# Kernel optimization log

Measured on AMD Instinct MI355X. Metric: run time of the kernel, lower is better.

## Reference

```python
import jax, jax.numpy as jnp
import numpy as np

N, T, H, D = 32, 2048, 1024, 384

def setup_inputs() -> dict:
    key = jax.random.key(0)
    k1, k2, k3, k4, k5 = jax.random.split(key, 5)
    scale_h = 1.0 / np.sqrt(H)
    scale_d = 1.0 / np.sqrt(D)
    return {
        "gru_output": jax.random.normal(k1, (N, T, H), dtype=jnp.float32),
        "condition": jax.random.normal(k2, (N, D), dtype=jnp.float32),
        "W_h": jax.random.normal(k3, (H, H), dtype=jnp.float32) * scale_h,
        "W_c": jax.random.normal(k4, (D, H), dtype=jnp.float32) * scale_d,
        "bias": jnp.zeros((H,), dtype=jnp.float32),
        "v": jax.random.normal(k5, (H,), dtype=jnp.float32) * scale_h,
    }

def reference(gru_output, condition, W_h, W_c, bias, v):
    # h_proj: (N, T, H); c_proj: (N, 1, H)
    h_proj = jnp.einsum("nth,hk->ntk", gru_output, W_h)
    c_proj = jnp.einsum("nd,dk->nk", condition, W_c)[:, None, :]
    energy = jnp.tanh(h_proj + c_proj + bias)          # (N, T, H)
    scores = jnp.einsum("ntk,k->nt", energy, v)        # (N, T)
    weights = jax.nn.softmax(scores, axis=-1)          # (N, T)
    context = jnp.einsum("nth,nt->nh", gru_output, weights)  # (N, H)
    return context
```

## Files before the change

### kernel.cpp

```cpp
#include <hip/hip_runtime.h>
#include <hip/hip_bf16.h>

#define N_B 32
#define T_S 2048
#define H_D 1024
#define D_C 384
#define NT  (N_B * T_S)

typedef __attribute__((ext_vector_type(8))) short bf16x8;
typedef __attribute__((ext_vector_type(4))) float f32x4;

__device__ __forceinline__ ushort f2bf(float f) {
    union { float f; unsigned u; } x; x.f = f;
    unsigned u = x.u;
    unsigned r = (u + 0x7FFFu + ((u >> 16) & 1u)) >> 16;
    return (ushort)r;
}

__device__ __forceinline__ float fast_tanh(float x) {
    float e = __expf(2.0f * x);
    return 1.0f - 2.0f / (e + 1.0f);
}

__global__ __launch_bounds__(256) void transpose_kernel(
    const float* __restrict__ W, ushort* __restrict__ Wt)
{
    __shared__ ushort tile[64 * 66];
    const int bx = blockIdx.x & 15;
    const int by = blockIdx.x >> 4;
    const int t = threadIdx.x;
    #pragma unroll
    for (int i = 0; i < 16; ++i) {
        int idx = t + i * 256;
        int r = idx >> 6, c = idx & 63;
        tile[r * 66 + c] = f2bf(W[(size_t)(by * 64 + r) * H_D + bx * 64 + c]);
    }
    __syncthreads();
    #pragma unroll
    for (int i = 0; i < 16; ++i) {
        int idx = t + i * 256;
        int r = idx >> 6, c = idx & 63;
        Wt[(size_t)(bx * 64 + r) * H_D + by * 64 + c] = tile[c * 66 + r];
    }
}

__global__ __launch_bounds__(256) void cproj_kernel(
    const float* __restrict__ cond, const float* __restrict__ Wc,
    const float* __restrict__ bias, float* __restrict__ cproj)
{
    const int idx = blockIdx.x * 256 + threadIdx.x;
    const int n = idx >> 10, k = idx & 1023;
    float acc = bias[k];
    const float* cp = cond + n * D_C;
    for (int d = 0; d < D_C; ++d)
        acc = fmaf(cp[d], Wc[(size_t)d * H_D + k], acc);
    cproj[idx] = acc;
}

#define LDSS 40
__global__ __launch_bounds__(256) void gemm_score_kernel(
    const float* __restrict__ gru, const ushort* __restrict__ Wt,
    const float* __restrict__ cproj, const float* __restrict__ v,
    float* __restrict__ scores)
{
    __shared__ __align__(16) ushort As[128 * LDSS];
    __shared__ __align__(16) ushort Bt[128 * LDSS];
    const int kb = blockIdx.x;
    const int mb = blockIdx.y;
    const int m0 = mb * 128;
    const int nbatch = mb >> 4;
    const int t = threadIdx.x;
    const int lane = t & 63, wave = t >> 6;
    const int wm = wave & 1, wn = wave >> 1;
    const int q = lane >> 4, ln = lane & 15;

    f32x4 acc[4][4];
    #pragma unroll
    for (int i = 0; i < 4; ++i)
        #pragma unroll
        for (int j = 0; j < 4; ++j)
            acc[i][j] = (f32x4){0.f, 0.f, 0.f, 0.f};

    for (int h0 = 0; h0 < H_D; h0 += 32) {
        if (h0) __syncthreads();
        #pragma unroll
        for (int i = 0; i < 4; ++i) {
            int f = t + i * 256;
            int row = f >> 3, c4 = f & 7;
            const float4 val = *(const float4*)(gru + (size_t)(m0 + row) * H_D + h0 + c4 * 4);
            ushort4 o;
            o.x = f2bf(val.x); o.y = f2bf(val.y); o.z = f2bf(val.z); o.w = f2bf(val.w);
            *(ushort4*)(&As[row * LDSS + c4 * 4]) = o;
        }
        #pragma unroll
        for (int i = 0; i < 2; ++i) {
            int f = t + i * 256;
            int n = f >> 2, c = f & 3;
            uint4 wv = *(const uint4*)(Wt + (size_t)(kb * 128 + n) * H_D + h0 + c * 8);
            *(uint4*)(&Bt[n * LDSS + c * 8]) = wv;
        }
        __syncthreads();
        bf16x8 a[4], b[4];
        #pragma unroll
        for (int i = 0; i < 4; ++i)
            a[i] = *(const bf16x8*)(&As[(wm * 64 + i * 16 + ln) * LDSS + q * 8]);
        #pragma unroll
        for (int j = 0; j < 4; ++j)
            b[j] = *(const bf16x8*)(&Bt[(wn * 64 + j * 16 + ln) * LDSS + q * 8]);
        #pragma unroll
        for (int i = 0; i < 4; ++i)
            #pragma unroll
            for (int j = 0; j < 4; ++j)
                acc[i][j] = __builtin_amdgcn_mfma_f32_16x16x32_bf16(a[i], b[j], acc[i][j], 0, 0, 0);
    }

    float cpv[4], vv[4];
    const float* cpn = cproj + nbatch * H_D;
    #pragma unroll
    for (int j = 0; j < 4; ++j) {
        int col = kb * 128 + wn * 64 + j * 16 + ln;
        cpv[j] = cpn[col];
        vv[j] = v[col];
    }
    #pragma unroll
    for (int i = 0; i < 4; ++i) {
        float s0 = 0.f, s1 = 0.f, s2 = 0.f, s3 = 0.f;
        #pragma unroll
        for (int j = 0; j < 4; ++j) {
            s0 += fast_tanh(acc[i][j][0] + cpv[j]) * vv[j];
            s1 += fast_tanh(acc[i][j][1] + cpv[j]) * vv[j];
            s2 += fast_tanh(acc[i][j][2] + cpv[j]) * vv[j];
            s3 += fast_tanh(acc[i][j][3] + cpv[j]) * vv[j];
        }
        #pragma unroll
        for (int off = 1; off < 16; off <<= 1) {
            s0 += __shfl_xor(s0, off);
            s1 += __shfl_xor(s1, off);
            s2 += __shfl_xor(s2, off);
            s3 += __shfl_xor(s3, off);
        }
        if (ln == 0) {
            int mrow = m0 + wm * 64 + i * 16 + q * 4;
            atomicAdd(&scores[mrow + 0], s0);
            atomicAdd(&scores[mrow + 1], s1);
            atomicAdd(&scores[mrow + 2], s2);
            atomicAdd(&scores[mrow + 3], s3);
        }
    }
}

__global__ __launch_bounds__(256) void softmax_kernel(
    const float* __restrict__ scores, float* __restrict__ weights)
{
    const int n = blockIdx.x;
    const int t = threadIdx.x;
    __shared__ float red[256];
    float sv[8];
    float m = -1e30f;
    #pragma unroll
    for (int i = 0; i < 8; ++i) {
        sv[i] = scores[n * T_S + i * 256 + t];
        m = fmaxf(m, sv[i]);
    }
    red[t] = m; __syncthreads();
    for (int s = 128; s > 0; s >>= 1) {
        if (t < s) red[t] = fmaxf(red[t], red[t + s]);
        __syncthreads();
    }
    const float mx = red[0];
    __syncthreads();
    float sum = 0.f;
    #pragma unroll
    for (int i = 0; i < 8; ++i) { sv[i] = __expf(sv[i] - mx); sum += sv[i]; }
    red[t] = sum; __syncthreads();
    for (int s = 128; s > 0; s >>= 1) {
        if (t < s) red[t] += red[t + s];
        __syncthreads();
    }
    const float inv = 1.0f / red[0];
    #pragma unroll
    for (int i = 0; i < 8; ++i) weights[n * T_S + i * 256 + t] = sv[i] * inv;
}

__global__ __launch_bounds__(256) void context_kernel(
    const float* __restrict__ gru, const float* __restrict__ weights,
    float* __restrict__ out)
{
    const int tb = blockIdx.x;
    const int n  = blockIdx.y;
    const int t4 = threadIdx.x;
    float4 acc = make_float4(0.f, 0.f, 0.f, 0.f);
    const float* wp = weights + n * T_S + tb * 256;
    const float* gp = gru + (size_t)(n * T_S + tb * 256) * H_D + t4 * 4;
    for (int tt = 0; tt < 256; ++tt) {
        float w = wp[tt];
        float4 gv = *(const float4*)(gp + (size_t)tt * H_D);
        acc.x += w * gv.x; acc.y += w * gv.y;
        acc.z += w * gv.z; acc.w += w * gv.w;
    }
    float* op = out + n * H_D + t4 * 4;
    atomicAdd(op + 0, acc.x);
    atomicAdd(op + 1, acc.y);
    atomicAdd(op + 2, acc.z);
    atomicAdd(op + 3, acc.w);
}

extern "C" void kernel_launch(void* const* d_in, const int* in_sizes, int n_in,
                              void* d_out, int out_size, void* d_ws, size_t ws_size,
                              hipStream_t stream)
{
    const float* gru  = (const float*)d_in[0];
    const float* cond = (const float*)d_in[1];
    const float* W_h  = (const float*)d_in[2];
    const float* W_c  = (const float*)d_in[3];
    const float* bias = (const float*)d_in[4];
    const float* v    = (const float*)d_in[5];
    float* out = (float*)d_out;

    char* ws = (char*)d_ws;
    ushort* Wt     = (ushort*)ws;
    float*  cproj  = (float*)(ws + (2u << 20));
    float*  scores = (float*)(ws + (2u << 20) + (128u << 10));
    float*  wts    = (float*)(ws + (2u << 20) + (384u << 10));

    hipMemsetAsync(scores, 0, NT * sizeof(float), stream);
    hipMemsetAsync(out, 0, N_B * H_D * sizeof(float), stream);

    transpose_kernel<<<256, 256, 0, stream>>>(W_h, Wt);
    cproj_kernel<<<128, 256, 0, stream>>>(cond, W_c, bias, cproj);
    gemm_score_kernel<<<dim3(8, 512), 256, 0, stream>>>(gru, Wt, cproj, v, scores);
    softmax_kernel<<<N_B, 256, 0, stream>>>(scores, wts);
    context_kernel<<<dim3(8, N_B), 256, 0, stream>>>(gru, wts, out);
}
```

Measured before the change: 650.6 us.

## Pre-convert activations to bf16 and load GEMM tiles directly into LDS

Adds a pass that converts gru_output to bf16 once into the workspace. The GEMM then streams both operands with global_load_lds straight into shared memory, so the fp32 data is no longer re-read and re-converted by every one of the 8 column blocks. Per-block score partials go to separate slices that the softmax kernel sums, replacing the atomics and the memset. The cost is an extra full read and write of the activations plus a 128 MB workspace requirement; without that workspace the code falls back to the old path. The unpadded LDS layout may also cause bank conflicts.

```diff
diff --git a/kernel.cpp b/kernel.cpp
--- a/kernel.cpp
+++ b/kernel.cpp
@@ -9,6 +9,7 @@
 
 typedef __attribute__((ext_vector_type(8))) short bf16x8;
 typedef __attribute__((ext_vector_type(4))) float f32x4;
+typedef __attribute__((ext_vector_type(8))) unsigned short u16x8;
 
 __device__ __forceinline__ ushort f2bf(float f) {
     union { float f; unsigned u; } x; x.f = f;
@@ -22,6 +23,24 @@
     return 1.0f - 2.0f / (e + 1.0f);
 }
 
+__device__ __forceinline__ void gl2lds16(const void* g, void* l) {
+    __builtin_amdgcn_global_load_lds(
+        (const __attribute__((address_space(1))) void*)g,
+        (__attribute__((address_space(3))) void*)l, 16, 0, 0);
+}
+
+__global__ __launch_bounds__(256) void convert_kernel(
+    const float* __restrict__ g, ushort* __restrict__ gb)
+{
+    const size_t base = ((size_t)blockIdx.x * 256 + threadIdx.x) * 8;
+    float4 v0 = *(const float4*)(g + base);
+    float4 v1 = *(const float4*)(g + base + 4);
+    u16x8 o;
+    o[0] = f2bf(v0.x); o[1] = f2bf(v0.y); o[2] = f2bf(v0.z); o[3] = f2bf(v0.w);
+    o[4] = f2bf(v1.x); o[5] = f2bf(v1.y); o[6] = f2bf(v1.z); o[7] = f2bf(v1.w);
+    *(u16x8*)(gb + base) = o;
+}
+
 __global__ __launch_bounds__(256) void transpose_kernel(
     const float* __restrict__ W, ushort* __restrict__ Wt)
 {
@@ -50,11 +69,110 @@
 {
     const int idx = blockIdx.x * 256 + threadIdx.x;
     const int n = idx >> 10, k = idx & 1023;
-    float acc = bias[k];
+    float a0 = bias[k], a1 = 0.f, a2 = 0.f, a3 = 0.f;
     const float* cp = cond + n * D_C;
-    for (int d = 0; d < D_C; ++d)
-        acc = fmaf(cp[d], Wc[(size_t)d * H_D + k], acc);
-    cproj[idx] = acc;
+    for (int d = 0; d < D_C; d += 4) {
+        a0 = fmaf(cp[d + 0], Wc[(size_t)(d + 0) * H_D + k], a0);
+        a1 = fmaf(cp[d + 1], Wc[(size_t)(d + 1) * H_D + k], a1);
+        a2 = fmaf(cp[d + 2], Wc[(size_t)(d + 2) * H_D + k], a2);
+        a3 = fmaf(cp[d + 3], Wc[(size_t)(d + 3) * H_D + k], a3);
+    }
+    cproj[idx] = (a0 + a1) + (a2 + a3);
+}
+
+__global__ __launch_bounds__(256) void gemm2_kernel(
+    const ushort* __restrict__ Ab, const ushort* __restrict__ Wt,
+    const float* __restrict__ cproj, const float* __restrict__ v,
+    float* __restrict__ spart)
+{
+    __shared__ __align__(16) ushort As[128 * 32];
+    __shared__ __align__(16) ushort Bs[128 * 32];
+    __shared__ float red[2][2][4][16];
+    const int kb = blockIdx.x;
+    const int mb = blockIdx.y;
+    const int m0 = mb * 128;
+    const int nbatch = mb >> 4;
+    const int t = threadIdx.x;
+    const int lane = t & 63, wave = t >> 6;
+    const int wm = wave & 1, wn = wave >> 1;
+    const int q = lane >> 4, ln = lane & 15;
+
+    const ushort* ag0 = Ab + (size_t)(m0 + (t >> 2)) * H_D + (t & 3) * 8;
+    const ushort* ag1 = Ab + (size_t)(m0 + 64 + (t >> 2)) * H_D + (t & 3) * 8;
+    const ushort* bg0 = Wt + (size_t)(kb * 128 + (t >> 2)) * H_D + (t & 3) * 8;
+    const ushort* bg1 = Wt + (size_t)(kb * 128 + 64 + (t >> 2)) * H_D + (t & 3) * 8;
+    ushort* asd0 = As + wave * 512;
+    ushort* asd1 = As + 2048 + wave * 512;
+    ushort* bsd0 = Bs + wave * 512;
+    ushort* bsd1 = Bs + 2048 + wave * 512;
+
+    f32x4 acc[4][4];
+    #pragma unroll
+    for (int i = 0; i < 4; ++i)
+        #pragma unroll
+        for (int j = 0; j < 4; ++j)
+            acc[i][j] = (f32x4){0.f, 0.f, 0.f, 0.f};
+
+    for (int h0 = 0; h0 < H_D; h0 += 32) {
+        if (h0) __syncthreads();
+        gl2lds16(ag0 + h0, asd0);
+        gl2lds16(ag1 + h0, asd1);
+        gl2lds16(bg0 + h0, bsd0);
+        gl2lds16(bg1 + h0, bsd1);
+        __syncthreads();
+        bf16x8 a[4], b[4];
+        #pragma unroll
+        for (int i = 0; i < 4; ++i)
+            a[i] = *(const bf16x8*)(&As[(wm * 64 + i * 16 + ln) * 32 + q * 8]);
+        #pragma unroll
+        for (int j = 0; j < 4; ++j)
+            b[j] = *(const bf16x8*)(&Bs[(wn * 64 + j * 16 + ln) * 32 + q * 8]);
+        #pragma unroll
+        for (int i = 0; i < 4; ++i)
+            #pragma unroll
+            for (int j = 0; j < 4; ++j)
+                acc[i][j] = __builtin_amdgcn_mfma_f32_16x16x32_bf16(a[i], b[j], acc[i][j], 0, 0, 0);
+    }
+
+    float cpv[4], vv[4];
+    const float* cpn = cproj + nbatch * H_D;
+    #pragma unroll
+    for (int j = 0; j < 4; ++j) {
+        int col = kb * 128 + wn * 64 + j * 16 + ln;
+        cpv[j] = cpn[col];
+        vv[j] = v[col];
+    }
+    #pragma unroll
+    for (int i = 0; i < 4; ++i) {
+        float s0 = 0.f, s1 = 0.f, s2 = 0.f, s3 = 0.f;
+        #pragma unroll
+        for (int j = 0; j < 4; ++j) {
+            s0 += fast_tanh(acc[i][j][0] + cpv[j]) * vv[j];
+            s1 += fast_tanh(acc[i][j][1] + cpv[j]) * vv[j];
+            s2 += fast_tanh(acc[i][j][2] + cpv[j]) * vv[j];
+            s3 += fast_tanh(acc[i][j][3] + cpv[j]) * vv[j];
+        }
+        #pragma unroll
+        for (int off = 1; off < 16; off <<= 1) {
+            s0 += __shfl_xor(s0, off);
+            s1 += __shfl_xor(s1, off);
+            s2 += __shfl_xor(s2, off);
+            s3 += __shfl_xor(s3, off);
+        }
+        if (ln == 0) {
+            red[wm][wn][i][q * 4 + 0] = s0;
+            red[wm][wn][i][q * 4 + 1] = s1;
+            red[wm][wn][i][q * 4 + 2] = s2;
+            red[wm][wn][i][q * 4 + 3] = s3;
+        }
+    }
+    __syncthreads();
+    if (t < 128) {
+        int wm2 = t >> 6, idx = t & 63;
+        int i2 = idx >> 4, qr = idx & 15;
+        float val = red[wm2][0][i2][qr] + red[wm2][1][i2][qr];
+        spart[(size_t)kb * NT + m0 + wm2 * 64 + idx] = val;
+    }
 }
 
 #define LDSS 40
@@ -147,6 +265,43 @@
             atomicAdd(&scores[mrow + 3], s3);
         }
     }
+}
+
+__global__ __launch_bounds__(256) void softmax8_kernel(
+    const float* __restrict__ spart, float* __restrict__ weights)
+{
+    const int n = blockIdx.x;
+    const int t = threadIdx.x;
+    __shared__ float red[256];
+    float sv[8];
+    float m = -1e30f;
+    #pragma unroll
+    for (int i = 0; i < 8; ++i) {
+        int mrow = n * T_S + i * 256 + t;
+        float s = 0.f;
+        #pragma unroll
+        for (int kb = 0; kb < 8; ++kb) s += spart[(size_t)kb * NT + mrow];
+        sv[i] = s;
+        m = fmaxf(m, s);
+    }
+    red[t] = m; __syncthreads();
+    for (int s = 128; s > 0; s >>= 1) {
+        if (t < s) red[t] = fmaxf(red[t], red[t + s]);
+        __syncthreads();
+    }
+    const float mx = red[0];
+    __syncthreads();
+    float sum = 0.f;
+    #pragma unroll
+    for (int i = 0; i < 8; ++i) { sv[i] = __expf(sv[i] - mx); sum += sv[i]; }
+    red[t] = sum; __syncthreads();
+    for (int s = 128; s > 0; s >>= 1) {
+        if (t < s) red[t] += red[t + s];
+        __syncthreads();
+    }
+    const float inv = 1.0f / red[0];
+    #pragma unroll
+    for (int i = 0; i < 8; ++i) weights[n * T_S + i * 256 + t] = sv[i] * inv;
 }
 
 __global__ __launch_bounds__(256) void softmax_kernel(
@@ -218,17 +373,39 @@
     float* out = (float*)d_out;
 
     char* ws = (char*)d_ws;
-    ushort* Wt     = (ushort*)ws;
-    float*  cproj  = (float*)(ws + (2u << 20));
-    float*  scores = (float*)(ws + (2u << 20) + (128u << 10));
-    float*  wts    = (float*)(ws + (2u << 20) + (384u << 10));
-
-    hipMemsetAsync(scores, 0, NT * sizeof(float), stream);
-    hipMemsetAsync(out, 0, N_B * H_D * sizeof(float), stream);
-
-    transpose_kernel<<<256, 256, 0, stream>>>(W_h, Wt);
-    cproj_kernel<<<128, 256, 0, stream>>>(cond, W_c, bias, cproj);
-    gemm_score_kernel<<<dim3(8, 512), 256, 0, stream>>>(gru, Wt, cproj, v, scores);
-    softmax_kernel<<<N_B, 256, 0, stream>>>(scores, wts);
-    context_kernel<<<dim3(8, N_B), 256, 0, stream>>>(gru, wts, out);
-}
+    const size_t szAb    = (size_t)NT * H_D * 2;
+    const size_t szWt    = (size_t)H_D * H_D * 2;
+    const size_t szCproj = (size_t)N_B * H_D * 4;
+    const size_t szSpart = (size_t)8 * NT * 4;
+    const size_t szWts   = (size_t)NT * 4;
+    const size_t need = szAb + szWt + szCproj + szSpart + szWts;
+
+    if (ws_size >= need) {
+        ushort* Ab    = (ushort*)ws;
+        ushort* Wt    = (ushort*)(ws + szAb);
+        float* cproj  = (float*)(ws + szAb + szWt);
+        float* spart  = (float*)(ws + szAb + szWt + szCproj);
+        float* wts    = (float*)(ws + szAb + szWt + szCproj + szSpart);
+
+        hipMemsetAsync(out, 0, N_B * H_D * sizeof(float), stream);
+        convert_kernel<<<32768, 256, 0, stream>>>(gru, Ab);
+        transpose_kernel<<<256, 256, 0, stream>>>(W_h, Wt);
+        cproj_kernel<<<128, 256, 0, stream>>>(cond, W_c, bias, cproj);
+        gemm2_kernel<<<dim3(8, 512), 256, 0, stream>>>(Ab, Wt, cproj, v, spart);
+        softmax8_kernel<<<N_B, 256, 0, stream>>>(spart, wts);
+        context_kernel<<<dim3(8, N_B), 256, 0, stream>>>(gru, wts, out);
+    } else {
+        ushort* Wt    = (ushort*)ws;
+        float* cproj  = (float*)(ws + szWt);
+        float* scores = (float*)(ws + szWt + szCproj);
+        float* wts    = (float*)(ws + szWt + szCproj + (size_t)NT * 4);
+
+        hipMemsetAsync(scores, 0, NT * sizeof(float), stream);
+        hipMemsetAsync(out, 0, N_B * H_D * sizeof(float), stream);
+        transpose_kernel<<<256, 256, 0, stream>>>(W_h, Wt);
+        cproj_kernel<<<128, 256, 0, stream>>>(cond, W_c, bias, cproj);
+        gemm_score_kernel<<<dim3(8, 512), 256, 0, stream>>>(gru, Wt, cproj, v, scores);
+        softmax_kernel<<<N_B, 256, 0, stream>>>(scores, wts);
+        context_kernel<<<dim3(8, N_B), 256, 0, stream>>>(gru, wts, out);
+    }
+}
```

Result: faster. 634.8 us (-2.4%).
